# Performance work log

Measured on AMD Instinct MI355X. Metric: run time of the kernel, lower is better.

## Reference

```python
import jax, jax.numpy as jnp
import numpy as np

B, H, K = 8192, 1024, 512


def setup_inputs() -> dict:
    key = jax.random.key(0)
    ks = jax.random.split(key, 7)
    return {
        "encoder_final_state": jax.random.normal(ks[0], (B, H), jnp.float32),
        "W_mu": (jax.random.normal(ks[1], (H, H), jnp.float32) * 0.02),
        "b_mu": jnp.zeros((H,), jnp.float32),
        "W_ls": (jax.random.normal(ks[2], (H, H), jnp.float32) * 0.02),
        "b_ls": jnp.zeros((H,), jnp.float32),
        "mu_c": jax.random.normal(ks[3], (K, H), jnp.float32),
        "log_sigma_sq_c": jax.random.normal(ks[4], (K, H), jnp.float32) * 0.1,
        "eps_z": jax.random.normal(ks[5], (B, H), jnp.float32),
    }


def reference(encoder_final_state, W_mu, b_mu, W_ls, b_ls, mu_c, log_sigma_sq_c, eps_z):
    x = encoder_final_state                      # [B,H]
    mu_z = x @ W_mu.T + b_mu                     # [B,H]
    ls_z = x @ W_ls.T + b_ls                     # [B,H] log sigma^2 of z
    z = mu_z + jnp.exp(0.5 * ls_z) * eps_z       # reparameterized sample [B,H]

    inv_sig = jnp.exp(-log_sigma_sq_c)           # [K,H] 1/sigma_c^2
    mu_inv = mu_c * inv_sig                      # [K,H]
    c2 = jnp.sum(mu_c * mu_inv, axis=-1)         # [K]

    def mahal(v):
        # sum_h (v - mu_c)^2 / sigma_c^2, expanded quadratic -> [B,K] via GEMMs
        return (v * v) @ inv_sig.T - 2.0 * (v @ mu_inv.T) + c2[None, :]

    att = jax.nn.softmax(-mahal(z), axis=-1)     # [B,K] cluster assignment

    # avg_ = mean_h( log_sigma_c + exp(ls_z)/sigma_c + (mu_z - mu_c)^2/sigma_c )
    avg_ = (jnp.sum(log_sigma_sq_c, axis=-1)[None, :]
            + jnp.exp(ls_z) @ inv_sig.T
            + mahal(mu_z)) / H                   # [B,K]
    sum_ = jnp.sum(att * avg_, axis=-1)          # [B]
    mean_ = jnp.mean(1.0 + ls_z, axis=-1)        # [B]
    batch_latent_loss = 0.5 * sum_ - 0.5 * mean_ # [B]

    cate_mean = jnp.mean(att, axis=0)            # [K]
    batch_cate_loss = jnp.mean(cate_mean * jnp.log(cate_mean))  # scalar
    return z, batch_latent_loss, batch_cate_loss
```

## Files before the change

kernel.cpp:

```cpp
#include <hip/hip_runtime.h>

#define BB 8192
#define HH 1024
#define KK 512

typedef __bf16 bf16x8 __attribute__((ext_vector_type(8)));
typedef __bf16 bf16x4 __attribute__((ext_vector_type(4)));
typedef float  f32x4  __attribute__((ext_vector_type(4)));

#define GLOAD_LDS16(gptr, lptr)                                                   \
  __builtin_amdgcn_global_load_lds((const __attribute__((address_space(1))) void*)(gptr), \
                                   (__attribute__((address_space(3))) void*)(lptr), 16, 0, 0)

static __device__ __forceinline__ void split_bf16(float f, __bf16& hi, __bf16& lo) {
  hi = (__bf16)f;
  lo = (__bf16)(f - (float)hi);
}

__global__ __launch_bounds__(256) void p1_split(const float* __restrict__ x,
                                                __bf16* __restrict__ xh,
                                                __bf16* __restrict__ xl) {
  const size_t i = ((size_t)blockIdx.x * 256 + threadIdx.x) * 4;
  const float4 v = *(const float4*)(x + i);
  float f[4] = {v.x, v.y, v.z, v.w};
  bf16x4 hv, lv;
#pragma unroll
  for (int j = 0; j < 4; ++j) {
    __bf16 h, l; split_bf16(f[j], h, l);
    hv[j] = h; lv[j] = l;
  }
  *(bf16x4*)(xh + i) = hv;
  *(bf16x4*)(xl + i) = lv;
}

__global__ __launch_bounds__(256) void p2_w1(const float* __restrict__ Wmu,
                                             const float* __restrict__ Wls,
                                             __bf16* __restrict__ W1p) {
  const int j = blockIdx.y;
  const int k = blockIdx.x * 256 + threadIdx.x;
  const int g = j >> 7, o = j & 127;
  const int n = o >> 4, o16 = o & 15;
  const int c = g * 64 + (n >> 1) * 16 + o16;
  const float* src = (n & 1) ? Wls : Wmu;
  const int ch = k >> 10, h = k & 1023;
  const float f = src[(size_t)c * 1024 + h];
  __bf16 hi, lo; split_bf16(f, hi, lo);
  W1p[(size_t)j * 3072 + k] = (ch == 1) ? lo : hi;
}

__global__ __launch_bounds__(256) void p3_cluster(const float* __restrict__ muc,
                                                  const float* __restrict__ lsc,
                                                  __bf16* __restrict__ W2p,
                                                  float* __restrict__ c2,
                                                  float* __restrict__ logdet,
                                                  float* __restrict__ acc) {
  const int k = blockIdx.x;
  const int t = threadIdx.x;
  if (t == 0) acc[k] = 0.f;
  float c2acc = 0.f, ldacc = 0.f;
  const size_t rb = (size_t)k * 4096;
#pragma unroll
  for (int i = 0; i < 4; ++i) {
    const int h = t + i * 256;
    const float l = lsc[(size_t)k * 1024 + h];
    const float m = muc[(size_t)k * 1024 + h];
    const float inv = expf(-l);
    const float mi = m * inv;
    c2acc += m * mi;
    ldacc += l;
    __bf16 h0, l0, h1, l1;
    split_bf16(inv, h0, l0);
    split_bf16(-2.f * mi, h1, l1);
    W2p[rb + h]        = h0; W2p[rb + 1024 + h] = h1;
    W2p[rb + 2048 + h] = l0; W2p[rb + 3072 + h] = l1;
  }
#pragma unroll
  for (int off = 32; off; off >>= 1) {
    c2acc += __shfl_down(c2acc, off);
    ldacc += __shfl_down(ldacc, off);
  }
  __shared__ float r4[8];
  if ((t & 63) == 0) { r4[(t >> 6)] = c2acc; r4[4 + (t >> 6)] = ldacc; }
  __syncthreads();
  if (t == 0) {
    c2[k]     = r4[0] + r4[1] + r4[2] + r4[3];
    logdet[k] = r4[4] + r4[5] + r4[6] + r4[7];
  }
}

__global__ __launch_bounds__(256, 2) void gemm1z(const __bf16* __restrict__ Ah,
                                                 const __bf16* __restrict__ Al,
                                                 const __bf16* __restrict__ W,
                                                 const float* __restrict__ bmu,
                                                 const float* __restrict__ bls,
                                                 const float* __restrict__ eps,
                                                 float* __restrict__ z_out,
                                                 __bf16* __restrict__ Az,
                                                 __bf16* __restrict__ Aq,
                                                 float* __restrict__ lss) {
  __shared__ __align__(16) __bf16 ldsA[2][128 * 64];
  __shared__ __align__(16) __bf16 ldsB[2][128 * 64];

  const int t = threadIdx.x;
  const int wv = t >> 6, lane = t & 63;
  const int l15 = lane & 15, l4 = lane >> 4;
  const int wr = wv >> 1, wc = wv & 1;
  const int bm0 = blockIdx.x * 128;
  const int bn0 = blockIdx.y * 128;
  const int g = blockIdx.y;

  f32x4 acc[4][4] = {};

  auto stage = [&](int k0, int b) {
    const int chunk = k0 >> 10;
    const int kin = k0 & 1023;
    const __bf16* Abase = (chunk == 2) ? Al : Ah;
#pragma unroll
    for (int i = 0; i < 4; ++i) {
      const int obase = i * 4096 + wv * 1024;
      const int o = obase + lane * 16;
      const int row = o >> 7;
      const int cb = o & 127;
      const int cbs = cb ^ ((row & 7) << 4);
      GLOAD_LDS16(Abase + (size_t)(bm0 + row) * 1024 + kin + (cbs >> 1), (char*)ldsA[b] + obase);
      GLOAD_LDS16(W + (size_t)(bn0 + row) * 3072 + k0 + (cbs >> 1), (char*)ldsB[b] + obase);
    }
  };

  stage(0, 0);
  __syncthreads();
  int cur = 0;

  for (int tt = 0; tt < 48; ++tt) {
    if (tt < 47) stage((tt + 1) * 64, cur ^ 1);

#pragma unroll
    for (int kkk = 0; kkk < 2; ++kkk) {
      bf16x8 av[4], bv[4];
#pragma unroll
      for (int m = 0; m < 4; ++m) {
        const int row = wr * 64 + m * 16 + l15;
        const int cb = kkk * 64 + l4 * 16;
        av[m] = *(const bf16x8*)((const char*)ldsA[cur] + row * 128 + (cb ^ ((row & 7) << 4)));
      }
#pragma unroll
      for (int n = 0; n < 4; ++n) {
        const int row = wc * 64 + n * 16 + l15;
        const int cb = kkk * 64 + l4 * 16;
        bv[n] = *(const bf16x8*)((const char*)ldsB[cur] + row * 128 + (cb ^ ((row & 7) << 4)));
      }
#pragma unroll
      for (int m = 0; m < 4; ++m)
#pragma unroll
        for (int n = 0; n < 4; ++n)
          acc[m][n] = __builtin_amdgcn_mfma_f32_16x16x32_bf16(av[m], bv[n], acc[m][n], 0, 0, 0);
    }
    __syncthreads();
    cur ^= 1;
  }

  float lsum[4][4];
#pragma unroll
  for (int m = 0; m < 4; ++m)
#pragma unroll
    for (int j = 0; j < 4; ++j) lsum[m][j] = 0.f;

#pragma unroll
  for (int pr = 0; pr < 2; ++pr) {
    const int h = g * 64 + (wc * 2 + pr) * 16 + l15;
    const float bm_v = bmu[h];
    const float bl_v = bls[h];
#pragma unroll
    for (int m = 0; m < 4; ++m) {
#pragma unroll
      for (int j = 0; j < 4; ++j) {
        const int row = bm0 + wr * 64 + m * 16 + l4 * 4 + j;
        const float mu = acc[m][2 * pr][j] + bm_v;
        const float ls = acc[m][2 * pr + 1][j] + bl_v;
        const float e = eps[(size_t)row * 1024 + h];
        const float sh = expf(0.5f * ls);
        const float z = fmaf(sh, e, mu);
        z_out[(size_t)row * 1024 + h] = z;
        Az[(size_t)row * 2048 + h]        = (__bf16)(z * z);
        Az[(size_t)row * 2048 + 1024 + h] = (__bf16)z;
        Aq[(size_t)row * 2048 + h]        = (__bf16)fmaf(mu, mu, sh * sh);
        Aq[(size_t)row * 2048 + 1024 + h] = (__bf16)mu;
        lsum[m][j] += ls;
      }
    }
  }
#pragma unroll
  for (int m = 0; m < 4; ++m) {
#pragma unroll
    for (int j = 0; j < 4; ++j) {
      float v = lsum[m][j];
      v += __shfl_xor(v, 1); v += __shfl_xor(v, 2);
      v += __shfl_xor(v, 4); v += __shfl_xor(v, 8);
      if (l15 == 0)
        atomicAdd(&lss[bm0 + wr * 64 + m * 16 + l4 * 4 + j], v);
    }
  }
}

__global__ __launch_bounds__(256, 2) void gemm2_fly(const __bf16* __restrict__ Az,
                                                    const __bf16* __restrict__ Aq,
                                                    const float* __restrict__ zbuf,
                                                    const __bf16* __restrict__ W2,
                                                    float* __restrict__ Cpart) {
  const int jb = blockIdx.z;
  float* Cc = Cpart + (size_t)jb * BB * KK;
  const int bcol = (jb == 1) ? 2048 : 0;
  const __bf16* Asrc = (jb == 3) ? Aq : Az;

  __shared__ __align__(16) __bf16 ldsA[2][128 * 64];
  __shared__ __align__(16) __bf16 ldsB[2][128 * 64];

  const int t = threadIdx.x;
  const int wv = t >> 6, lane = t & 63;
  const int l15 = lane & 15, l4 = lane >> 4;
  const int wr = wv >> 1, wc = wv & 1;
  const int bm0 = blockIdx.x * 128;
  const int bn0 = blockIdx.y * 128;

  f32x4 acc[4][4] = {};

  auto stageB = [&](int k0, int b) {
#pragma unroll
    for (int i = 0; i < 4; ++i) {
      const int obase = i * 4096 + wv * 1024;
      const int o = obase + lane * 16;
      const int row = o >> 7;
      const int cb = o & 127;
      const int cbs = cb ^ ((row & 7) << 4);
      GLOAD_LDS16(W2 + (size_t)(bn0 + row) * 4096 + bcol + k0 + (cbs >> 1), (char*)ldsB[b] + obase);
    }
  };
  auto stageA_g = [&](int k0, int b) {
#pragma unroll
    for (int i = 0; i < 4; ++i) {
      const int obase = i * 4096 + wv * 1024;
      const int o = obase + lane * 16;
      const int row = o >> 7;
      const int cb = o & 127;
      const int cbs = cb ^ ((row & 7) << 4);
      GLOAD_LDS16(Asrc + (size_t)(bm0 + row) * 2048 + k0 + (cbs >> 1), (char*)ldsA[b] + obase);
    }
  };
  auto ldA_issue = [&](int k0, float4 fa[4][2]) {
    const bool quad = k0 < 1024;
    const int hcol = quad ? k0 : (k0 - 1024);
#pragma unroll
    for (int v = 0; v < 4; ++v) {
      const int id = v * 256 + t;
      const int row = id >> 3;
      const int c8 = id & 7;
      const float* src = zbuf + (size_t)(bm0 + row) * 1024 + hcol + c8 * 8;
      fa[v][0] = *(const float4*)(src);
      fa[v][1] = *(const float4*)(src + 4);
    }
  };
  auto ldA_commit = [&](int k0, const float4 fa[4][2], int b) {
    const bool quad = k0 < 1024;
#pragma unroll
    for (int v = 0; v < 4; ++v) {
      const int id = v * 256 + t;
      const int row = id >> 3;
      const int c8 = id & 7;
      float vals[8] = {fa[v][0].x, fa[v][0].y, fa[v][0].z, fa[v][0].w,
                       fa[v][1].x, fa[v][1].y, fa[v][1].z, fa[v][1].w};
      if (quad) {
#pragma unroll
        for (int j = 0; j < 8; ++j) vals[j] = vals[j] * vals[j];
      }
      bf16x8 w;
#pragma unroll
      for (int j = 0; j < 8; ++j) {
        const __bf16 h = (__bf16)vals[j];
        w[j] = (__bf16)(vals[j] - (float)h);
      }
      const int cb = c8 * 16;
      *(bf16x8*)((char*)ldsA[b] + row * 128 + (cb ^ ((row & 7) << 4))) = w;
    }
  };

  if (jb == 2) {
    float4 fa[4][2];
    ldA_issue(0, fa);
    stageB(0, 0);
    ldA_commit(0, fa, 0);
  } else {
    stageA_g(0, 0);
    stageB(0, 0);
  }
  __syncthreads();
  int cur = 0;

  for (int tt = 0; tt < 32; ++tt) {
    const int k0n = (tt + 1) * 64;
    const bool pf = (tt < 31);
    float4 fa[4][2];
    if (pf) {
      if (jb == 2) ldA_issue(k0n, fa);
      else         stageA_g(k0n, cur ^ 1);
      stageB(k0n, cur ^ 1);
    }

#pragma unroll
    for (int kkk = 0; kkk < 2; ++kkk) {
      bf16x8 av[4], bv[4];
#pragma unroll
      for (int m = 0; m < 4; ++m) {
        const int row = wr * 64 + m * 16 + l15;
        const int cb = kkk * 64 + l4 * 16;
        av[m] = *(const bf16x8*)((const char*)ldsA[cur] + row * 128 + (cb ^ ((row & 7) << 4)));
      }
#pragma unroll
      for (int n = 0; n < 4; ++n) {
        const int row = wc * 64 + n * 16 + l15;
        const int cb = kkk * 64 + l4 * 16;
        bv[n] = *(const bf16x8*)((const char*)ldsB[cur] + row * 128 + (cb ^ ((row & 7) << 4)));
      }
#pragma unroll
      for (int m = 0; m < 4; ++m)
#pragma unroll
        for (int n = 0; n < 4; ++n)
          acc[m][n] = __builtin_amdgcn_mfma_f32_16x16x32_bf16(av[m], bv[n], acc[m][n], 0, 0, 0);
    }

    if (pf && jb == 2) ldA_commit(k0n, fa, cur ^ 1);
    __syncthreads();
    cur ^= 1;
  }

#pragma unroll
  for (int m = 0; m < 4; ++m) {
#pragma unroll
    for (int n = 0; n < 4; ++n) {
      const int gr0 = bm0 + wr * 64 + m * 16 + l4 * 4;
      const int gc  = bn0 + wc * 64 + n * 16 + l15;
#pragma unroll
      for (int j = 0; j < 4; ++j)
        Cc[(size_t)(gr0 + j) * 512 + gc] = acc[m][n][j];
    }
  }
}

__global__ __launch_bounds__(256) void k4_rows(const float* __restrict__ Cpart,
                                               const float* __restrict__ c2,
                                               const float* __restrict__ logdet,
                                               const float* __restrict__ ls_sum,
                                               float* __restrict__ out_loss,
                                               float* __restrict__ acc) {
  const float* S0 = Cpart;
  const float* S1 = Cpart + (size_t)BB * KK;
  const float* S2 = Cpart + (size_t)2 * BB * KK;
  const float* S3 = Cpart + (size_t)3 * BB * KK;
  const int t = threadIdx.x;
  const int wv = t >> 6, lane = t & 63;
  __shared__ float sacc[512];
  sacc[t] = 0.f; sacc[t + 256] = 0.f;
  __syncthreads();
  float c2r[8], avr[8], attsum[8];
#pragma unroll
  for (int i = 0; i < 8; ++i) {
    const int k = lane + i * 64;
    c2r[i] = c2[k];
    avr[i] = logdet[k] + c2r[i];
    attsum[i] = 0.f;
  }
  for (int r = 0; r < 8; ++r) {
    const int b = blockIdx.x * 32 + wv * 8 + r;
    const size_t rb = (size_t)b * 512;
    float mv[8], ev[8];
    float lm = 3.4e38f;
#pragma unroll
    for (int i = 0; i < 8; ++i) {
      const size_t idx = rb + lane + i * 64;
      mv[i] = S0[idx] + S1[idx] + S2[idx] + c2r[i];
      lm = fminf(lm, mv[i]);
    }
#pragma unroll
    for (int off = 32; off; off >>= 1) lm = fminf(lm, __shfl_xor(lm, off));
    float s = 0.f, dot = 0.f;
#pragma unroll
    for (int i = 0; i < 8; ++i) {
      const size_t idx = rb + lane + i * 64;
      const float e = expf(lm - mv[i]);
      const float avg = (avr[i] + S3[idx]) * (1.f / 1024.f);
      ev[i] = e;
      s += e;
      dot = fmaf(e, avg, dot);
    }
#pragma unroll
    for (int off = 32; off; off >>= 1) {
      s   += __shfl_xor(s, off);
      dot += __shfl_xor(dot, off);
    }
    const float inv_s = 1.f / s;
    if (lane == 0)
      out_loss[b] = 0.5f * (dot * inv_s) - 0.5f * (1.f + ls_sum[b] * (1.f / 1024.f));
#pragma unroll
    for (int i = 0; i < 8; ++i) attsum[i] += ev[i] * inv_s;
  }
#pragma unroll
  for (int i = 0; i < 8; ++i) atomicAdd(&sacc[lane + i * 64], attsum[i]);
  __syncthreads();
  atomicAdd(&acc[t], sacc[t]);
  atomicAdd(&acc[t + 256], sacc[t + 256]);
}

__global__ __launch_bounds__(512) void k6_final(const float* __restrict__ acc,
                                                float* __restrict__ out) {
  const int t = threadIdx.x;
  const float cm = acc[t] * (1.f / 8192.f);
  float v = cm * logf(cm);
#pragma unroll
  for (int off = 32; off; off >>= 1) v += __shfl_xor(v, off);
  __shared__ float r8[8];
  if ((t & 63) == 0) r8[t >> 6] = v;
  __syncthreads();
  if (t == 0) {
    float s = 0.f;
#pragma unroll
    for (int i = 0; i < 8; ++i) s += r8[i];
    out[0] = s * (1.f / 512.f);
  }
}

extern "C" void kernel_launch(void* const* d_in, const int* in_sizes, int n_in,
                              void* d_out, int out_size, void* d_ws, size_t ws_size,
                              hipStream_t stream) {
  const float* x   = (const float*)d_in[0];
  const float* Wmu = (const float*)d_in[1];
  const float* bmu = (const float*)d_in[2];
  const float* Wls = (const float*)d_in[3];
  const float* bls = (const float*)d_in[4];
  const float* muc = (const float*)d_in[5];
  const float* lsc = (const float*)d_in[6];
  const float* eps = (const float*)d_in[7];
  float* out = (float*)d_out;

  char* p = (char*)d_ws;
  auto carve = [&](size_t bytes) {
    char* r = p;
    p += (bytes + 255) & ~(size_t)255;
    return r;
  };
  __bf16* Az  = (__bf16*)carve((size_t)BB * 2048 * 2);
  __bf16* Aq  = (__bf16*)carve((size_t)BB * 2048 * 2);
  __bf16* W2p = (__bf16*)carve((size_t)KK * 4096 * 2);
  float*  c2v = (float*) carve(KK * 4);
  float*  ldv = (float*) carve(KK * 4);
  float*  lss = (float*) carve(BB * 4);
  float*  acc = (float*) carve(KK * 4);
  char* uni = carve((size_t)4 * BB * KK * 4);
  __bf16* xh  = (__bf16*)uni;
  __bf16* xl  = (__bf16*)(uni + (size_t)BB * HH * 2);
  __bf16* W1p = (__bf16*)(uni + (size_t)BB * HH * 4);
  float*  Cpart = (float*)uni;

  float* z_out    = out;
  float* loss_out = out + (size_t)BB * HH;
  float* cate_out = loss_out + BB;

  hipMemsetAsync(lss, 0, BB * sizeof(float), stream);

  p1_split<<<dim3(BB * HH / 1024), 256, 0, stream>>>(x, xh, xl);
  p2_w1<<<dim3(12, 2048), 256, 0, stream>>>(Wmu, Wls, W1p);
  p3_cluster<<<dim3(KK), 256, 0, stream>>>(muc, lsc, W2p, c2v, ldv, acc);

  gemm1z<<<dim3(BB / 128, 2048 / 128), 256, 0, stream>>>(xh, xl, W1p, bmu, bls, eps,
                                                         z_out, Az, Aq, lss);

  gemm2_fly<<<dim3(BB / 128, KK / 128, 4), 256, 0, stream>>>(Az, Aq, z_out, W2p, Cpart);

  k4_rows<<<dim3(BB / 32), 256, 0, stream>>>(Cpart, c2v, ldv, lss, loss_out, acc);
  k6_final<<<dim3(1), 512, 0, stream>>>(acc, cate_out);
}
```

Baseline: 396.7 us.

## Single-buffer LDS in GEMMs to raise occupancy and fold lss zeroing

```diff
diff --git a/kernel.cpp b/kernel.cpp
--- a/kernel.cpp
+++ b/kernel.cpp
@@ -53,10 +53,12 @@
                                                   __bf16* __restrict__ W2p,
                                                   float* __restrict__ c2,
                                                   float* __restrict__ logdet,
-                                                  float* __restrict__ acc) {
+                                                  float* __restrict__ acc,
+                                                  float* __restrict__ lss) {
   const int k = blockIdx.x;
   const int t = threadIdx.x;
   if (t == 0) acc[k] = 0.f;
+  if (t < 16) lss[k * 16 + t] = 0.f;
   float c2acc = 0.f, ldacc = 0.f;
   const size_t rb = (size_t)k * 4096;
 #pragma unroll
@@ -88,7 +90,7 @@
   }
 }
 
-__global__ __launch_bounds__(256, 2) void gemm1z(const __bf16* __restrict__ Ah,
+__global__ __launch_bounds__(256, 3) void gemm1z(const __bf16* __restrict__ Ah,
                                                  const __bf16* __restrict__ Al,
                                                  const __bf16* __restrict__ W,
                                                  const float* __restrict__ bmu,
@@ -98,8 +100,8 @@
                                                  __bf16* __restrict__ Az,
                                                  __bf16* __restrict__ Aq,
                                                  float* __restrict__ lss) {
-  __shared__ __align__(16) __bf16 ldsA[2][128 * 64];
-  __shared__ __align__(16) __bf16 ldsB[2][128 * 64];
+  __shared__ __align__(16) __bf16 ldsA[128 * 64];
+  __shared__ __align__(16) __bf16 ldsB[128 * 64];
 
   const int t = threadIdx.x;
   const int wv = t >> 6, lane = t & 63;
@@ -111,7 +113,8 @@
 
   f32x4 acc[4][4] = {};
 
-  auto stage = [&](int k0, int b) {
+  for (int tt = 0; tt < 48; ++tt) {
+    const int k0 = tt * 64;
     const int chunk = k0 >> 10;
     const int kin = k0 & 1023;
     const __bf16* Abase = (chunk == 2) ? Al : Ah;
@@ -122,17 +125,10 @@
       const int row = o >> 7;
       const int cb = o & 127;
       const int cbs = cb ^ ((row & 7) << 4);
-      GLOAD_LDS16(Abase + (size_t)(bm0 + row) * 1024 + kin + (cbs >> 1), (char*)ldsA[b] + obase);
-      GLOAD_LDS16(W + (size_t)(bn0 + row) * 3072 + k0 + (cbs >> 1), (char*)ldsB[b] + obase);
-    }
-  };
-
-  stage(0, 0);
-  __syncthreads();
-  int cur = 0;
-
-  for (int tt = 0; tt < 48; ++tt) {
-    if (tt < 47) stage((tt + 1) * 64, cur ^ 1);
+      GLOAD_LDS16(Abase + (size_t)(bm0 + row) * 1024 + kin + (cbs >> 1), (char*)ldsA + obase);
+      GLOAD_LDS16(W + (size_t)(bn0 + row) * 3072 + k0 + (cbs >> 1), (char*)ldsB + obase);
+    }
+    __syncthreads();
 
 #pragma unroll
     for (int kkk = 0; kkk < 2; ++kkk) {
@@ -141,13 +137,13 @@
       for (int m = 0; m < 4; ++m) {
         const int row = wr * 64 + m * 16 + l15;
         const int cb = kkk * 64 + l4 * 16;
-        av[m] = *(const bf16x8*)((const char*)ldsA[cur] + row * 128 + (cb ^ ((row & 7) << 4)));
+        av[m] = *(const bf16x8*)((const char*)ldsA + row * 128 + (cb ^ ((row & 7) << 4)));
       }
 #pragma unroll
       for (int n = 0; n < 4; ++n) {
         const int row = wc * 64 + n * 16 + l15;
         const int cb = kkk * 64 + l4 * 16;
-        bv[n] = *(const bf16x8*)((const char*)ldsB[cur] + row * 128 + (cb ^ ((row & 7) << 4)));
+        bv[n] = *(const bf16x8*)((const char*)ldsB + row * 128 + (cb ^ ((row & 7) << 4)));
       }
 #pragma unroll
       for (int m = 0; m < 4; ++m)
@@ -156,7 +152,6 @@
           acc[m][n] = __builtin_amdgcn_mfma_f32_16x16x32_bf16(av[m], bv[n], acc[m][n], 0, 0, 0);
     }
     __syncthreads();
-    cur ^= 1;
   }
 
   float lsum[4][4];
@@ -202,7 +197,7 @@
   }
 }
 
-__global__ __launch_bounds__(256, 2) void gemm2_fly(const __bf16* __restrict__ Az,
+__global__ __launch_bounds__(256, 3) void gemm2_fly(const __bf16* __restrict__ Az,
                                                     const __bf16* __restrict__ Aq,
                                                     const float* __restrict__ zbuf,
                                                     const __bf16* __restrict__ W2,
@@ -212,8 +207,8 @@
   const int bcol = (jb == 1) ? 2048 : 0;
   const __bf16* Asrc = (jb == 3) ? Aq : Az;
 
-  __shared__ __align__(16) __bf16 ldsA[2][128 * 64];
-  __shared__ __align__(16) __bf16 ldsB[2][128 * 64];
+  __shared__ __align__(16) __bf16 ldsA[128 * 64];
+  __shared__ __align__(16) __bf16 ldsB[128 * 64];
 
   const int t = threadIdx.x;
   const int wv = t >> 6, lane = t & 63;
@@ -224,7 +219,7 @@
 
   f32x4 acc[4][4] = {};
 
-  auto stageB = [&](int k0, int b) {
+  auto stageB = [&](int k0) {
 #pragma unroll
     for (int i = 0; i < 4; ++i) {
       const int obase = i * 4096 + wv * 1024;
@@ -232,10 +227,10 @@
       const int row = o >> 7;
       const int cb = o & 127;
       const int cbs = cb ^ ((row & 7) << 4);
-      GLOAD_LDS16(W2 + (size_t)(bn0 + row) * 4096 + bcol + k0 + (cbs >> 1), (char*)ldsB[b] + obase);
+      GLOAD_LDS16(W2 + (size_t)(bn0 + row) * 4096 + bcol + k0 + (cbs >> 1), (char*)ldsB + obase);
     }
   };
-  auto stageA_g = [&](int k0, int b) {
+  auto stageA_g = [&](int k0) {
 #pragma unroll
     for (int i = 0; i < 4; ++i) {
       const int obase = i * 4096 + wv * 1024;
@@ -243,7 +238,7 @@
       const int row = o >> 7;
       const int cb = o & 127;
       const int cbs = cb ^ ((row & 7) << 4);
-      GLOAD_LDS16(Asrc + (size_t)(bm0 + row) * 2048 + k0 + (cbs >> 1), (char*)ldsA[b] + obase);
+      GLOAD_LDS16(Asrc + (size_t)(bm0 + row) * 2048 + k0 + (cbs >> 1), (char*)ldsA + obase);
     }
   };
   auto ldA_issue = [&](int k0, float4 fa[4][2]) {
@@ -259,7 +254,7 @@
       fa[v][1] = *(const float4*)(src + 4);
     }
   };
-  auto ldA_commit = [&](int k0, const float4 fa[4][2], int b) {
+  auto ldA_commit = [&](int k0, const float4 fa[4][2]) {
     const bool quad = k0 < 1024;
 #pragma unroll
     for (int v = 0; v < 4; ++v) {
@@ -279,31 +274,22 @@
         w[j] = (__bf16)(vals[j] - (float)h);
       }
       const int cb = c8 * 16;
-      *(bf16x8*)((char*)ldsA[b] + row * 128 + (cb ^ ((row & 7) << 4))) = w;
+      *(bf16x8*)((char*)ldsA + row * 128 + (cb ^ ((row & 7) << 4))) = w;
     }
   };
 
-  if (jb == 2) {
-    float4 fa[4][2];
-    ldA_issue(0, fa);
-    stageB(0, 0);
-    ldA_commit(0, fa, 0);
-  } else {
-    stageA_g(0, 0);
-    stageB(0, 0);
-  }
-  __syncthreads();
-  int cur = 0;
+  float4 fa[4][2];
+  if (jb == 2) ldA_issue(0, fa);
 
   for (int tt = 0; tt < 32; ++tt) {
-    const int k0n = (tt + 1) * 64;
-    const bool pf = (tt < 31);
-    float4 fa[4][2];
-    if (pf) {
-      if (jb == 2) ldA_issue(k0n, fa);
-      else         stageA_g(k0n, cur ^ 1);
-      stageB(k0n, cur ^ 1);
-    }
+    const int k0 = tt * 64;
+    if (jb == 2) ldA_commit(k0, fa);
+    else         stageA_g(k0);
+    stageB(k0);
+    __syncthreads();
+
+    if (jb == 2 && tt + 1 < 32)
+      ldA_issue((tt + 1) * 64, fa);
 
 #pragma unroll
     for (int kkk = 0; kkk < 2; ++kkk) {
@@ -312,13 +298,13 @@
       for (int m = 0; m < 4; ++m) {
         const int row = wr * 64 + m * 16 + l15;
         const int cb = kkk * 64 + l4 * 16;
-        av[m] = *(const bf16x8*)((const char*)ldsA[cur] + row * 128 + (cb ^ ((row & 7) << 4)));
+        av[m] = *(const bf16x8*)((const char*)ldsA + row * 128 + (cb ^ ((row & 7) << 4)));
       }
 #pragma unroll
       for (int n = 0; n < 4; ++n) {
         const int row = wc * 64 + n * 16 + l15;
         const int cb = kkk * 64 + l4 * 16;
-        bv[n] = *(const bf16x8*)((const char*)ldsB[cur] + row * 128 + (cb ^ ((row & 7) << 4)));
+        bv[n] = *(const bf16x8*)((const char*)ldsB + row * 128 + (cb ^ ((row & 7) << 4)));
       }
 #pragma unroll
       for (int m = 0; m < 4; ++m)
@@ -326,10 +312,7 @@
         for (int n = 0; n < 4; ++n)
           acc[m][n] = __builtin_amdgcn_mfma_f32_16x16x32_bf16(av[m], bv[n], acc[m][n], 0, 0, 0);
     }
-
-    if (pf && jb == 2) ldA_commit(k0n, fa, cur ^ 1);
     __syncthreads();
-    cur ^= 1;
   }
 
 #pragma unroll
@@ -463,11 +446,9 @@
   float* loss_out = out + (size_t)BB * HH;
   float* cate_out = loss_out + BB;
 
-  hipMemsetAsync(lss, 0, BB * sizeof(float), stream);
-
   p1_split<<<dim3(BB * HH / 1024), 256, 0, stream>>>(x, xh, xl);
   p2_w1<<<dim3(12, 2048), 256, 0, stream>>>(Wmu, Wls, W1p);
-  p3_cluster<<<dim3(KK), 256, 0, stream>>>(muc, lsc, W2p, c2v, ldv, acc);
+  p3_cluster<<<dim3(KK), 256, 0, stream>>>(muc, lsc, W2p, c2v, ldv, acc, lss);
 
   gemm1z<<<dim3(BB / 128, 2048 / 128), 256, 0, stream>>>(xh, xl, W1p, bmu, bls, eps,
                                                          z_out, Az, Aq, lss);
```

Measured after the change: 452.4 us. 1.14x slower.
